# Optimization experiments

Hardware: AMD Instinct MI355X
Metric: run time of the kernel (lower is better)

The kernel has to match this reference:

```python
import jax, jax.numpy as jnp
import numpy as np

B = 4096
D_INPUT = 20
CTX = 10
IN_DIM = CTX * (D_INPUT + 1) + D_INPUT  # 230
D_MODEL = 256
N_LAYERS = 12
D_STATE = 16
D_CONV = 4
EXPAND = 2
D_INNER = EXPAND * D_MODEL  # 512
DT_RANK = (D_MODEL + 15) // 16  # ceil(256/16) = 16


def setup_inputs() -> dict:
    key = jax.random.key(0)
    ks = jax.random.split(key, 12)
    s = lambda k, shape, scale=0.02: jax.random.normal(k, shape, jnp.float32) * scale
    A = jnp.broadcast_to(jnp.arange(1, D_STATE + 1, dtype=jnp.float32), (N_LAYERS, D_INNER, D_STATE))
    return {
        "x": jax.random.normal(ks[0], (B, IN_DIM), jnp.float32),
        "Wi": s(ks[1], (IN_DIM, D_MODEL)),
        "bi": jnp.zeros((D_MODEL,), jnp.float32),
        "in_proj_w": s(ks[2], (N_LAYERS, D_MODEL, 2 * D_INNER)),
        "conv_w": s(ks[3], (N_LAYERS, D_INNER, D_CONV), 0.3),
        "conv_b": jnp.zeros((N_LAYERS, D_INNER), jnp.float32),
        "x_proj_w": s(ks[4], (N_LAYERS, D_INNER, DT_RANK + 2 * D_STATE)),
        "dt_proj_w": s(ks[5], (N_LAYERS, DT_RANK, D_INNER), 0.1),
        "dt_proj_b": jnp.full((N_LAYERS, D_INNER), -4.6, jnp.float32),  # softplus -> small dt
        "A_log": jnp.log(A),  # S4D-real init as in mamba_ssm
        "D": jnp.ones((N_LAYERS, D_INNER), jnp.float32),
        "out_proj_w": s(ks[6], (N_LAYERS, D_INNER, D_MODEL)),
        "Wo": s(ks[7], (D_MODEL, 1)),
        "bo": jnp.zeros((1,), jnp.float32),
    }


def _mamba_block(h, in_proj, conv_w, conv_b, x_proj, dt_w, dt_b, A_log, Dp, out_proj):
    # h: (B, L, D_MODEL)
    Bn, L, _ = h.shape
    xz = h @ in_proj                       # (B, L, 2*D_INNER)
    xr, z = jnp.split(xz, 2, axis=-1)
    # causal depthwise conv1d, kernel D_CONV, left-pad D_CONV-1
    xp = jnp.pad(xr, ((0, 0), (D_CONV - 1, 0), (0, 0)))
    win = jnp.stack([xp[:, k:k + L, :] for k in range(D_CONV)], axis=-1)  # (B,L,C,K)
    xc = jnp.einsum('blck,ck->blc', win, conv_w) + conv_b
    xc = jax.nn.silu(xc)
    dbl = xc @ x_proj                      # (B, L, DT_RANK + 2*D_STATE)
    dt, Bm, Cm = jnp.split(dbl, [DT_RANK, DT_RANK + D_STATE], axis=-1)
    dt = jax.nn.softplus(dt @ dt_w + dt_b)  # (B, L, D_INNER)
    A = -jnp.exp(A_log)                     # (D_INNER, D_STATE)
    dA = jnp.exp(dt[..., None] * A)                              # (B,L,di,ds)
    dBu = dt[..., None] * Bm[:, :, None, :] * xc[..., None]      # (B,L,di,ds)

    def step(hs, inp):
        dA_t, dBu_t, C_t = inp
        hs = dA_t * hs + dBu_t             # (B, di, ds)
        y_t = jnp.einsum('bds,bs->bd', hs, C_t)
        return hs, y_t

    h0 = jnp.zeros((Bn, D_INNER, D_STATE), h.dtype)
    _, ys = jax.lax.scan(step, h0, (dA.swapaxes(0, 1), dBu.swapaxes(0, 1), Cm.swapaxes(0, 1)))
    y = ys.swapaxes(0, 1)                  # (B, L, D_INNER)
    y = y + xc * Dp
    y = y * jax.nn.silu(z)
    return y @ out_proj                    # (B, L, D_MODEL)


def reference(x, Wi, bi, in_proj_w, conv_w, conv_b, x_proj_w, dt_proj_w, dt_proj_b, A_log, D, out_proj_w, Wo, bo):
    h = (x @ Wi + bi)[:, None, :]          # (B, 1, D_MODEL) -- unsqueeze(1)
    for i in range(N_LAYERS):
        h = _mamba_block(h, in_proj_w[i], conv_w[i], conv_b[i], x_proj_w[i],
                         dt_proj_w[i], dt_proj_b[i], A_log[i], D[i], out_proj_w[i])
    h = h[:, 0, :]                         # squeeze(1)
    return h @ Wo + bo                     # (B, 1)
```

## Files before the change

### kernel.cpp

```cpp
#include <hip/hip_runtime.h>
#include <hip/hip_fp8.h>
#include <math.h>

#define NB 4096
#define IN_D 230
#define DM 256
#define NL 12
#define DST 16
#define DI 512
#define DTR 16
#define XPN 48
#define XB 520
#define HB 264

typedef __attribute__((ext_vector_type(4))) float floatx4;
typedef __attribute__((ext_vector_type(2))) float floatx2;
typedef __attribute__((ext_vector_type(2))) long long2v;
typedef __attribute__((ext_vector_type(4))) int intx4;

__device__ __forceinline__ float silu_f(float x) {
    return x * __builtin_amdgcn_rcpf(1.0f + __expf(-x));
}
__device__ __forceinline__ float softplus_f(float x) {
    return (x > 20.0f) ? x : __logf(1.0f + __expf(x));
}

__device__ __forceinline__ unsigned char f2fp8(float x) {
#if __has_builtin(__builtin_amdgcn_cvt_pk_fp8_f32)
    return (unsigned char)(__builtin_amdgcn_cvt_pk_fp8_f32(x, x, 0, false) & 0xff);
#else
    __hip_fp8_e4m3 t(x); return (unsigned char)t.__x;
#endif
}
__device__ __forceinline__ float fp82f(unsigned char b) {
#if __has_builtin(__builtin_amdgcn_cvt_f32_fp8)
    return __builtin_amdgcn_cvt_f32_fp8((int)b, 0);
#else
    __hip_fp8_e4m3 t; t.__x = (__hip_fp8_storage_t)b; return (float)t;
#endif
}


__global__ __launch_bounds__(256) void conv_x(const float* __restrict__ x, unsigned char* __restrict__ xp) {
    int idx = blockIdx.x * 256 + threadIdx.x;
    int r = idx >> 8, k = idx & 255;
    float v = (k < IN_D) ? x[(size_t)r * IN_D + k] : 0.0f;
    xp[idx] = f2fp8(v);
}

__global__ __launch_bounds__(256) void pack_all(
    const float* __restrict__ Wi, const float* __restrict__ ip,
    const float* __restrict__ op, const float* __restrict__ xp,
    const float* __restrict__ dtw,
    const float* __restrict__ cw, const float* __restrict__ cb,
    const float* __restrict__ db, const float* __restrict__ Dv,
    unsigned char* __restrict__ WiT, unsigned char* __restrict__ ipT,
    unsigned char* __restrict__ opT, unsigned char* __restrict__ xpT,
    unsigned char* __restrict__ dtwP,
    floatx2* __restrict__ cwcb, floatx2* __restrict__ dbdv)
{
    __shared__ float tbuf[64][65];
    const int fid = blockIdx.x;

    if (fid < 1264) {
        const float* src; unsigned char* dst;
        int K, N, Kp, ngK, t;
        if (fid < 16) {
            src = Wi; dst = WiT; K = IN_D; N = DM; Kp = DM; ngK = 4; t = fid;
        } else if (fid < 784) {
            int local = fid - 16; int l = local >> 6; t = local & 63;
            K = DM; N = 2 * DI; Kp = DM; ngK = 4;
            src = ip + (size_t)l * K * N; dst = ipT + (size_t)l * (2 * DI) * Kp;
        } else if (fid < 1168) {
            int local = fid - 784; int l = local >> 5; t = local & 31;
            K = DI; N = DM; Kp = DI; ngK = 8;
            src = op + (size_t)l * K * N; dst = opT + (size_t)l * DM * Kp;
        } else {
            int local = fid - 1168; int l = local >> 3; t = local & 7;
            K = DI; N = XPN; Kp = DI; ngK = 8;
            src = xp + (size_t)l * K * N; dst = xpT + (size_t)l * 64 * Kp;
        }
        const int g = t % ngK, nb = t / ngK;
        const int k0 = g * 64, n0 = nb * 64;
        const int r = threadIdx.x >> 6, c = threadIdx.x & 63;
#pragma unroll
        for (int i = 0; i < 16; i++) {
            int kk = k0 + i * 4 + r;
            int nn = n0 + c;
            tbuf[i * 4 + r][c] = (kk < K && nn < N) ? src[(size_t)kk * N + nn] : 0.0f;
        }
        __syncthreads();
        const int cbi = threadIdx.x >> 6;
        const int lane = threadIdx.x & 63;
        const int q = lane >> 4, m16 = lane & 15;
        const int chunk = (nb * 4 + cbi) * ngK + g;
        union { unsigned char b[16]; intx4 v; } buf;
#pragma unroll
        for (int sub = 0; sub < 2; sub++)
#pragma unroll
            for (int byt = 0; byt < 8; byt++) {
                int k = sub * 32 + q * 8 + byt;
                int n = cbi * 16 + m16;
                buf.b[sub * 8 + byt] = f2fp8(tbuf[k][n]);
            }
        *(intx4*)(dst + (size_t)chunk * 1024 + lane * 16) = buf.v;
    } else if (fid < 2032) {
        int local = fid - 1264;
        int l = local >> 6, bx = local & 63;
        int idx = bx * 256 + threadIdx.x;
        int chunk = idx >> 9;
        int rr = idx & 511;
        int lane = rr >> 3, byt = rr & 7;
        int q = lane >> 4, m16 = lane & 15;
        int col = chunk * 16 + m16;
        int k = q * 8 + byt;
        float v = (k < DTR) ? dtw[(size_t)l * DTR * DI + (size_t)k * DI + col] : 0.0f;
        dtwP[(size_t)l * 16384 + idx] = f2fp8(v);
    } else if (fid < 2056) {
        int idx = (fid - 2032) * 256 + threadIdx.x;
        floatx2 v; v.x = cw[(size_t)idx * 4 + 3]; v.y = cb[idx];
        cwcb[idx] = v;
    } else {
        int idx = (fid - 2056) * 256 + threadIdx.x;
        floatx2 v; v.x = db[idx]; v.y = Dv[idx];
        dbdv[idx] = v;
    }
}

__global__ __launch_bounds__(1024) void mamba_all(
    const unsigned char* __restrict__ xpad, const unsigned char* __restrict__ WiT,
    const float* __restrict__ bi,
    const unsigned char* __restrict__ ipT, const unsigned char* __restrict__ opT,
    const unsigned char* __restrict__ xpT, const unsigned char* __restrict__ dtwP,
    const floatx2* __restrict__ cwcb, const floatx2* __restrict__ dbdv,
    const float* __restrict__ Wo, const float* __restrict__ bo,
    float* __restrict__ out)
{
    __shared__ unsigned char hs[16 * HB];
    __shared__ unsigned char xcs[16 * XB];
    __shared__ unsigned char szs[16 * XB];
    __shared__ float dbls[16 * 68];

    const int tid = threadIdx.x;
    const int w = tid >> 6, lane = tid & 63;
    const int q = lane >> 4, m16 = lane & 15;
    const int rb = blockIdx.x * 16;

    {
        floatx4 a0 = (floatx4){0.f, 0.f, 0.f, 0.f};
        floatx4 a1 = (floatx4){0.f, 0.f, 0.f, 0.f};
        const unsigned char* Ap = xpad + (size_t)(rb + m16) * DM + q * 8;
        const unsigned char* Bp = WiT + (size_t)(w * 4) * 1024 + lane * 16;
#pragma unroll
        for (int g = 0; g < 4; g++) {
            long2v b = *(const long2v*)(Bp + g * 1024);
            long av0 = *(const long*)(Ap + (g * 2) * 32);
            long av1 = *(const long*)(Ap + (g * 2 + 1) * 32);
            a0 = __builtin_amdgcn_mfma_f32_16x16x32_fp8_fp8(av0, b.x, a0, 0, 0, 0);
            a1 = __builtin_amdgcn_mfma_f32_16x16x32_fp8_fp8(av1, b.y, a1, 0, 0, 0);
        }
        a0 = a0 + a1;
        int col = w * 16 + m16;
#pragma unroll
        for (int r = 0; r < 4; r++)
            hs[(q * 4 + r) * HB + col] = f2fp8(a0[r] + bi[col]);
    }
    __syncthreads();

    for (int l = 0; l < NL; l++) {
        const unsigned char* ip = ipT + (size_t)l * 2 * DI * DM;
        const unsigned char* xp = xpT + (size_t)l * 64 * DI;
        const unsigned char* op = opT + (size_t)l * DM * DI;
        const unsigned char* dwp = dtwP + (size_t)l * 16384;
        const floatx2* cc = cwcb + (size_t)l * DI;
        const floatx2* dd = dbdv + (size_t)l * DI;

        {
            floatx4 acc[4];
#pragma unroll
            for (int t = 0; t < 4; t++) acc[t] = (floatx4){0.f, 0.f, 0.f, 0.f};
            const unsigned char* Bp = ip + (size_t)(w * 16) * 1024 + lane * 16;
            const unsigned char* Ar = hs + m16 * HB + q * 8;
#pragma unroll
            for (int g = 0; g < 4; g++) {
                long a0 = *(const long*)(Ar + (g * 2) * 32);
                long a1 = *(const long*)(Ar + (g * 2 + 1) * 32);
                long2v b[4];
#pragma unroll
                for (int t = 0; t < 4; t++)
                    b[t] = *(const long2v*)(Bp + (size_t)(t * 4 + g) * 1024);
#pragma unroll
                for (int t = 0; t < 4; t++)
                    acc[t] = __builtin_amdgcn_mfma_f32_16x16x32_fp8_fp8(a0, b[t].x, acc[t], 0, 0, 0);
#pragma unroll
                for (int t = 0; t < 4; t++)
                    acc[t] = __builtin_amdgcn_mfma_f32_16x16x32_fp8_fp8(a1, b[t].y, acc[t], 0, 0, 0);
            }
            if (w < 8) {
#pragma unroll
                for (int t = 0; t < 4; t++) {
                    int col = w * 64 + t * 16 + m16;
                    floatx2 c2 = cc[col];
#pragma unroll
                    for (int r = 0; r < 4; r++) {
                        float v = silu_f(acc[t][r] * c2.x + c2.y);
                        xcs[(q * 4 + r) * XB + col] = f2fp8(v);
                    }
                }
            } else {
#pragma unroll
                for (int t = 0; t < 4; t++)
#pragma unroll
                    for (int r = 0; r < 4; r++) {
                        int col = (w - 8) * 64 + t * 16 + m16;
                        szs[(q * 4 + r) * XB + col] = f2fp8(silu_f(acc[t][r]));
                    }
            }
        }
        __syncthreads();

        if (w < 4) {
            floatx4 a0 = (floatx4){0.f, 0.f, 0.f, 0.f};
            floatx4 a1 = (floatx4){0.f, 0.f, 0.f, 0.f};
            const unsigned char* Bp = xp + (size_t)(w * 8) * 1024 + lane * 16;
            const unsigned char* Ar = xcs + m16 * XB + q * 8;
#pragma unroll
            for (int g = 0; g < 8; g++) {
                long2v b = *(const long2v*)(Bp + g * 1024);
                long av0 = *(const long*)(Ar + (g * 2) * 32);
                long av1 = *(const long*)(Ar + (g * 2 + 1) * 32);
                a0 = __builtin_amdgcn_mfma_f32_16x16x32_fp8_fp8(av0, b.x, a0, 0, 0, 0);
                a1 = __builtin_amdgcn_mfma_f32_16x16x32_fp8_fp8(av1, b.y, a1, 0, 0, 0);
            }
            a0 = a0 + a1;
#pragma unroll
            for (int r = 0; r < 4; r++)
                dbls[(q * 4 + r) * 68 + w * 16 + m16] = a0[r];
        }
        __syncthreads();

        {
            const unsigned char* Wp = dwp + (size_t)(w * 2) * 512 + lane * 8;
            long b0 = *(const long*)(Wp);
            long b1 = *(const long*)(Wp + 512);
            const int c0 = w * 32 + m16, c1 = c0 + 16;
            const floatx2 dd0 = dd[c0], dd1 = dd[c1];

            const int brow = lane >> 2, bj = lane & 3;
            const float* dr0 = &dbls[brow * 68 + DTR];
            float p = dr0[bj]      * dr0[DST + bj]
                    + dr0[bj + 4]  * dr0[DST + bj + 4]
                    + dr0[bj + 8]  * dr0[DST + bj + 8]
                    + dr0[bj + 12] * dr0[DST + bj + 12];
            p += __shfl_xor(p, 1);
            p += __shfl_xor(p, 2);
            float bcr[4];
#pragma unroll
            for (int r = 0; r < 4; r++) bcr[r] = __shfl(p, (q * 4 + r) * 4);

            long afrag = 0;
            if (q < 2) {
                const float* dr = &dbls[m16 * 68 + q * 8];
                unsigned lo, hi;
                lo = __builtin_amdgcn_cvt_pk_fp8_f32(dr[0], dr[1], 0, false);
                lo = __builtin_amdgcn_cvt_pk_fp8_f32(dr[2], dr[3], lo, true);
                hi = __builtin_amdgcn_cvt_pk_fp8_f32(dr[4], dr[5], 0, false);
                hi = __builtin_amdgcn_cvt_pk_fp8_f32(dr[6], dr[7], hi, true);
                union { unsigned u[2]; long l; } av;
                av.u[0] = lo; av.u[1] = hi;
                afrag = av.l;
            }
            floatx4 d0v = (floatx4){dd0.x, dd0.x, dd0.x, dd0.x};
            floatx4 d1v = (floatx4){dd1.x, dd1.x, dd1.x, dd1.x};
            d0v = __builtin_amdgcn_mfma_f32_16x16x32_fp8_fp8(afrag, b0, d0v, 0, 0, 0);
            d1v = __builtin_amdgcn_mfma_f32_16x16x32_fp8_fp8(afrag, b1, d1v, 0, 0, 0);
#pragma unroll
            for (int r = 0; r < 4; r++) {
                int row = q * 4 + r;
                int off0 = row * XB + c0;
                float v0 = (softplus_f(d0v[r]) * bcr[r] + dd0.y) * fp82f(xcs[off0]) * fp82f(szs[off0]);
                xcs[off0] = f2fp8(v0);
                int off1 = off0 + 16;
                float v1 = (softplus_f(d1v[r]) * bcr[r] + dd1.y) * fp82f(xcs[off1]) * fp82f(szs[off1]);
                xcs[off1] = f2fp8(v1);
            }
        }
        __syncthreads();

        {
            floatx4 a0 = (floatx4){0.f, 0.f, 0.f, 0.f};
            floatx4 a1 = (floatx4){0.f, 0.f, 0.f, 0.f};
            const unsigned char* Bp = op + (size_t)(w * 8) * 1024 + lane * 16;
            const unsigned char* Ar = xcs + m16 * XB + q * 8;
#pragma unroll
            for (int g = 0; g < 8; g++) {
                long2v b = *(const long2v*)(Bp + g * 1024);
                long av0 = *(const long*)(Ar + (g * 2) * 32);
                long av1 = *(const long*)(Ar + (g * 2 + 1) * 32);
                a0 = __builtin_amdgcn_mfma_f32_16x16x32_fp8_fp8(av0, b.x, a0, 0, 0, 0);
                a1 = __builtin_amdgcn_mfma_f32_16x16x32_fp8_fp8(av1, b.y, a1, 0, 0, 0);
            }
            a0 = a0 + a1;
            int col = w * 16 + m16;
#pragma unroll
            for (int r = 0; r < 4; r++)
                hs[(q * 4 + r) * HB + col] = f2fp8(a0[r]);
        }
        __syncthreads();
    }

    {
        float s = 0.0f;
#pragma unroll
        for (int j = 0; j < 4; j++)
            s += fp82f(hs[w * HB + lane * 4 + j]) * Wo[lane * 4 + j];
#pragma unroll
        for (int off = 32; off > 0; off >>= 1) s += __shfl_down(s, off);
        if (lane == 0) out[rb + w] = s + bo[0];
    }
}

extern "C" void kernel_launch(void* const* d_in, const int* in_sizes, int n_in,
                              void* d_out, int out_size, void* d_ws, size_t ws_size,
                              hipStream_t stream)
{
    const float* x       = (const float*)d_in[0];
    const float* Wi      = (const float*)d_in[1];
    const float* bi      = (const float*)d_in[2];
    const float* in_proj = (const float*)d_in[3];
    const float* conv_w  = (const float*)d_in[4];
    const float* conv_b  = (const float*)d_in[5];
    const float* x_proj  = (const float*)d_in[6];
    const float* dt_w    = (const float*)d_in[7];
    const float* dt_b    = (const float*)d_in[8];
    const float* Dp      = (const float*)d_in[10];
    const float* out_pw  = (const float*)d_in[11];
    const float* Wo      = (const float*)d_in[12];
    const float* bo      = (const float*)d_in[13];

    unsigned char* ws = (unsigned char*)d_ws;
    unsigned char* xpad = ws;
    unsigned char* WiT  = xpad + (size_t)NB * DM;
    unsigned char* ipT  = WiT + (size_t)DM * DM;
    unsigned char* opT  = ipT + (size_t)NL * 2 * DI * DM;
    unsigned char* xpT  = opT + (size_t)NL * DM * DI;
    unsigned char* dtwP = xpT + (size_t)NL * 64 * DI;
    floatx2* cwcb = (floatx2*)(dtwP + (size_t)NL * 16384);
    floatx2* dbdv = cwcb + (size_t)NL * DI;

    conv_x<<<dim3(NB * DM / 256), dim3(256), 0, stream>>>(x, xpad);
    pack_all<<<dim3(2080), dim3(256), 0, stream>>>(
        Wi, in_proj, out_pw, x_proj, dt_w, conv_w, conv_b, dt_b, Dp,
        WiT, ipT, opT, xpT, dtwP, cwcb, dbdv);

    mamba_all<<<dim3(NB / 16), dim3(1024), 0, stream>>>(
        xpad, WiT, bi, ipT, opT, xpT, dtwP,
        cwcb, dbdv, Wo, bo, (float*)d_out);
}
```

Measured before the change: 204.1 us.

## Quantize layer weights to FP4 and use scaled 16x16x128 MFMA

Adds a pack kernel that requantizes the FP8 in_proj, x_proj and out_proj weights into FP4 (E2M1) with a fixed power-of-two scale. The three per-layer GEMMs switch from the fp8 16x16x32 MFMA to the scaled 16x16x128 f8f6f4 MFMA with FP8 activations and FP4 weights. This roughly halves weight bytes and cuts the MFMA instruction count. LDS row padding changes to fit the wider 32-byte A-fragment loads. The cost is an extra pack launch and a large loss of weight precision that may break the accuracy tolerance.

```diff
diff --git a/kernel.cpp b/kernel.cpp
--- a/kernel.cpp
+++ b/kernel.cpp
@@ -10,13 +10,14 @@
 #define DI 512
 #define DTR 16
 #define XPN 48
-#define XB 520
-#define HB 264
+#define XB 528
+#define HB 272
 
 typedef __attribute__((ext_vector_type(4))) float floatx4;
 typedef __attribute__((ext_vector_type(2))) float floatx2;
 typedef __attribute__((ext_vector_type(2))) long long2v;
 typedef __attribute__((ext_vector_type(4))) int intx4;
+typedef __attribute__((ext_vector_type(8))) int intx8;
 
 __device__ __forceinline__ float silu_f(float x) {
     return x * __builtin_amdgcn_rcpf(1.0f + __expf(-x));
@@ -38,6 +39,21 @@
 #else
     __hip_fp8_e4m3 t; t.__x = (__hip_fp8_storage_t)b; return (float)t;
 #endif
+}
+
+__device__ __forceinline__ unsigned f2fp4(float x) {
+    float ax = fabsf(x);
+    unsigned s = (x < 0.0f) ? 8u : 0u;
+    unsigned m;
+    if      (ax < 0.25f) m = 0;
+    else if (ax < 0.75f) m = 1;
+    else if (ax < 1.25f) m = 2;
+    else if (ax < 1.75f) m = 3;
+    else if (ax < 2.50f) m = 4;
+    else if (ax < 3.50f) m = 5;
+    else if (ax < 5.00f) m = 6;
+    else                 m = 7;
+    return s | m;
 }
 
 
@@ -127,11 +143,51 @@
     }
 }
 
+__global__ __launch_bounds__(256) void pack_fp4(
+    const unsigned char* __restrict__ ipT, const unsigned char* __restrict__ opT,
+    const unsigned char* __restrict__ xpT,
+    unsigned char* __restrict__ ip4, unsigned char* __restrict__ op4,
+    unsigned char* __restrict__ xp4)
+{
+    const int fid = blockIdx.x;
+    const unsigned char* src8; unsigned char* dst4;
+    int nkg, ngK8, idx, lsz4, lsz8, l;
+    if (fid < 6144) {
+        l = fid >> 9; idx = (fid & 511) * 256 + threadIdx.x;
+        src8 = ipT; dst4 = ip4; nkg = 2; ngK8 = 4; lsz4 = 131072; lsz8 = 262144;
+    } else if (fid < 9216) {
+        int local = fid - 6144; l = local >> 8; idx = (local & 255) * 256 + threadIdx.x;
+        src8 = opT; dst4 = op4; nkg = 4; ngK8 = 8; lsz4 = 65536; lsz8 = 131072;
+    } else {
+        int local = fid - 9216; l = local >> 6; idx = (local & 63) * 256 + threadIdx.x;
+        src8 = xpT; dst4 = xp4; nkg = 4; ngK8 = 8; lsz4 = 16384; lsz8 = 32768;
+    }
+    src8 += (size_t)l * lsz8;
+    dst4 += (size_t)l * lsz4;
+
+    int chunk = idx >> 10;
+    int rem = idx & 1023;
+    int lane = rem >> 4, b = rem & 15;
+    int m16 = lane & 15, q4 = lane >> 4;
+    int cbk = chunk / nkg, kg = chunk - cbk * nkg;
+    unsigned outb = 0;
+#pragma unroll
+    for (int i = 0; i < 2; i++) {
+        int e = b * 2 + i;
+        int k = kg * 128 + q4 * 32 + e;
+        int g = k >> 6, sub = (k >> 5) & 1, q8 = (k >> 3) & 3, byt = k & 7;
+        size_t off8 = (size_t)(cbk * ngK8 + g) * 1024 + (q8 * 16 + m16) * 16 + sub * 8 + byt;
+        float v = fp82f(src8[off8]) * 128.0f;
+        outb |= f2fp4(v) << (i * 4);
+    }
+    dst4[idx] = (unsigned char)outb;
+}
+
 __global__ __launch_bounds__(1024) void mamba_all(
     const unsigned char* __restrict__ xpad, const unsigned char* __restrict__ WiT,
     const float* __restrict__ bi,
-    const unsigned char* __restrict__ ipT, const unsigned char* __restrict__ opT,
-    const unsigned char* __restrict__ xpT, const unsigned char* __restrict__ dtwP,
+    const unsigned char* __restrict__ ip4, const unsigned char* __restrict__ op4,
+    const unsigned char* __restrict__ xp4, const unsigned char* __restrict__ dtwP,
     const floatx2* __restrict__ cwcb, const floatx2* __restrict__ dbdv,
     const float* __restrict__ Wo, const float* __restrict__ bo,
     float* __restrict__ out)
@@ -145,6 +201,7 @@
     const int w = tid >> 6, lane = tid & 63;
     const int q = lane >> 4, m16 = lane & 15;
     const int rb = blockIdx.x * 16;
+    const long2v z2 = (long2v){0, 0};
 
     {
         floatx4 a0 = (floatx4){0.f, 0.f, 0.f, 0.f};
@@ -168,9 +225,9 @@
     __syncthreads();
 
     for (int l = 0; l < NL; l++) {
-        const unsigned char* ip = ipT + (size_t)l * 2 * DI * DM;
-        const unsigned char* xp = xpT + (size_t)l * 64 * DI;
-        const unsigned char* op = opT + (size_t)l * DM * DI;
+        const unsigned char* ip = ip4 + (size_t)l * 131072;
+        const unsigned char* xp = xp4 + (size_t)l * 16384;
+        const unsigned char* op = op4 + (size_t)l * 65536;
         const unsigned char* dwp = dtwP + (size_t)l * 16384;
         const floatx2* cc = cwcb + (size_t)l * DI;
         const floatx2* dd = dbdv + (size_t)l * DI;
@@ -179,22 +236,21 @@
             floatx4 acc[4];
 #pragma unroll
             for (int t = 0; t < 4; t++) acc[t] = (floatx4){0.f, 0.f, 0.f, 0.f};
-            const unsigned char* Bp = ip + (size_t)(w * 16) * 1024 + lane * 16;
-            const unsigned char* Ar = hs + m16 * HB + q * 8;
-#pragma unroll
-            for (int g = 0; g < 4; g++) {
-                long a0 = *(const long*)(Ar + (g * 2) * 32);
-                long a1 = *(const long*)(Ar + (g * 2 + 1) * 32);
-                long2v b[4];
-#pragma unroll
-                for (int t = 0; t < 4; t++)
-                    b[t] = *(const long2v*)(Bp + (size_t)(t * 4 + g) * 1024);
-#pragma unroll
-                for (int t = 0; t < 4; t++)
-                    acc[t] = __builtin_amdgcn_mfma_f32_16x16x32_fp8_fp8(a0, b[t].x, acc[t], 0, 0, 0);
-#pragma unroll
-                for (int t = 0; t < 4; t++)
-                    acc[t] = __builtin_amdgcn_mfma_f32_16x16x32_fp8_fp8(a1, b[t].y, acc[t], 0, 0, 0);
+            const unsigned char* Bp = ip + (size_t)(w * 8) * 1024 + lane * 16;
+            const unsigned char* Ar = hs + m16 * HB + q * 32;
+#pragma unroll
+            for (int kg = 0; kg < 2; kg++) {
+                union { long2v h[2]; intx8 v; } av;
+                av.h[0] = *(const long2v*)(Ar + kg * 128);
+                av.h[1] = *(const long2v*)(Ar + kg * 128 + 16);
+#pragma unroll
+                for (int t = 0; t < 4; t++) {
+                    union { long2v h[2]; intx8 v; } bv;
+                    bv.h[0] = *(const long2v*)(Bp + (size_t)(t * 2 + kg) * 1024);
+                    bv.h[1] = z2;
+                    acc[t] = __builtin_amdgcn_mfma_scale_f32_16x16x128_f8f6f4(
+                        av.v, bv.v, acc[t], 0, 4, 0, 127, 0, 120);
+                }
             }
             if (w < 8) {
 #pragma unroll
@@ -220,22 +276,23 @@
         __syncthreads();
 
         if (w < 4) {
-            floatx4 a0 = (floatx4){0.f, 0.f, 0.f, 0.f};
-            floatx4 a1 = (floatx4){0.f, 0.f, 0.f, 0.f};
-            const unsigned char* Bp = xp + (size_t)(w * 8) * 1024 + lane * 16;
-            const unsigned char* Ar = xcs + m16 * XB + q * 8;
-#pragma unroll
-            for (int g = 0; g < 8; g++) {
-                long2v b = *(const long2v*)(Bp + g * 1024);
-                long av0 = *(const long*)(Ar + (g * 2) * 32);
-                long av1 = *(const long*)(Ar + (g * 2 + 1) * 32);
-                a0 = __builtin_amdgcn_mfma_f32_16x16x32_fp8_fp8(av0, b.x, a0, 0, 0, 0);
-                a1 = __builtin_amdgcn_mfma_f32_16x16x32_fp8_fp8(av1, b.y, a1, 0, 0, 0);
-            }
-            a0 = a0 + a1;
+            floatx4 acc = (floatx4){0.f, 0.f, 0.f, 0.f};
+            const unsigned char* Bp = xp + (size_t)(w * 4) * 1024 + lane * 16;
+            const unsigned char* Ar = xcs + m16 * XB + q * 32;
+#pragma unroll
+            for (int kg = 0; kg < 4; kg++) {
+                union { long2v h[2]; intx8 v; } av;
+                av.h[0] = *(const long2v*)(Ar + kg * 128);
+                av.h[1] = *(const long2v*)(Ar + kg * 128 + 16);
+                union { long2v h[2]; intx8 v; } bv;
+                bv.h[0] = *(const long2v*)(Bp + (size_t)kg * 1024);
+                bv.h[1] = z2;
+                acc = __builtin_amdgcn_mfma_scale_f32_16x16x128_f8f6f4(
+                    av.v, bv.v, acc, 0, 4, 0, 127, 0, 120);
+            }
 #pragma unroll
             for (int r = 0; r < 4; r++)
-                dbls[(q * 4 + r) * 68 + w * 16 + m16] = a0[r];
+                dbls[(q * 4 + r) * 68 + w * 16 + m16] = acc[r];
         }
         __syncthreads();
 
@@ -288,23 +345,24 @@
         __syncthreads();
 
         {
-            floatx4 a0 = (floatx4){0.f, 0.f, 0.f, 0.f};
-            floatx4 a1 = (floatx4){0.f, 0.f, 0.f, 0.f};
-            const unsigned char* Bp = op + (size_t)(w * 8) * 1024 + lane * 16;
-            const unsigned char* Ar = xcs + m16 * XB + q * 8;
-#pragma unroll
-            for (int g = 0; g < 8; g++) {
-                long2v b = *(const long2v*)(Bp + g * 1024);
-                long av0 = *(const long*)(Ar + (g * 2) * 32);
-                long av1 = *(const long*)(Ar + (g * 2 + 1) * 32);
-                a0 = __builtin_amdgcn_mfma_f32_16x16x32_fp8_fp8(av0, b.x, a0, 0, 0, 0);
-                a1 = __builtin_amdgcn_mfma_f32_16x16x32_fp8_fp8(av1, b.y, a1, 0, 0, 0);
-            }
-            a0 = a0 + a1;
+            floatx4 acc = (floatx4){0.f, 0.f, 0.f, 0.f};
+            const unsigned char* Bp = op + (size_t)(w * 4) * 1024 + lane * 16;
+            const unsigned char* Ar = xcs + m16 * XB + q * 32;
+#pragma unroll
+            for (int kg = 0; kg < 4; kg++) {
+                union { long2v h[2]; intx8 v; } av;
+                av.h[0] = *(const long2v*)(Ar + kg * 128);
+                av.h[1] = *(const long2v*)(Ar + kg * 128 + 16);
+                union { long2v h[2]; intx8 v; } bv;
+                bv.h[0] = *(const long2v*)(Bp + (size_t)kg * 1024);
+                bv.h[1] = z2;
+                acc = __builtin_amdgcn_mfma_scale_f32_16x16x128_f8f6f4(
+                    av.v, bv.v, acc, 0, 4, 0, 127, 0, 120);
+            }
             int col = w * 16 + m16;
 #pragma unroll
             for (int r = 0; r < 4; r++)
-                hs[(q * 4 + r) * HB + col] = f2fp8(a0[r]);
+                hs[(q * 4 + r) * HB + col] = f2fp8(acc[r]);
         }
         __syncthreads();
     }
@@ -347,13 +405,18 @@
     unsigned char* dtwP = xpT + (size_t)NL * 64 * DI;
     floatx2* cwcb = (floatx2*)(dtwP + (size_t)NL * 16384);
     floatx2* dbdv = cwcb + (size_t)NL * DI;
+    unsigned char* ip4 = (unsigned char*)(dbdv + (size_t)NL * DI);
+    unsigned char* op4 = ip4 + (size_t)NL * 131072;
+    unsigned char* xp4 = op4 + (size_t)NL * 65536;
 
     conv_x<<<dim3(NB * DM / 256), dim3(256), 0, stream>>>(x, xpad);
     pack_all<<<dim3(2080), dim3(256), 0, stream>>>(
         Wi, in_proj, out_pw, x_proj, dt_w, conv_w, conv_b, dt_b, Dp,
         WiT, ipT, opT, xpT, dtwP, cwcb, dbdv);
+    pack_fp4<<<dim3(9984), dim3(256), 0, stream>>>(
+        ipT, opT, xpT, ip4, op4, xp4);
 
     mamba_all<<<dim3(NB / 16), dim3(1024), 0, stream>>>(
-        xpad, WiT, bi, ipT, opT, xpT, dtwP,
+        xpad, WiT, bi, ip4, op4, xp4, dtwP,
         cwcb, dbdv, Wo, bo, (float*)d_out);
 }
```

New measurement: 192.5 us. -5.7%, faster.
